# Kernel optimization log

Measured on AMD Instinct MI355X. Metric: run time of the kernel, lower is better.

Reference implementation:

```python
import jax, jax.numpy as jnp
import numpy as np

EPS = 1e-8  # torch F.cosine_similarity eps
TEMP = 1.0  # temperature k


def setup_inputs() -> dict:
    key = jax.random.key(0)
    k1, k2, k3 = jax.random.split(key, 3)
    B, T, N, D = 16, 4096, 512, 512
    c = jax.random.normal(k1, (B, T, D), dtype=jnp.float32)
    y_t = jax.random.normal(k2, (B, T, D), dtype=jnp.float32)
    y_distraction = jax.random.normal(k3, (B, N, D), dtype=jnp.float32)
    return {"c": c, "y_t": y_t, "y_distraction": y_distraction}


def reference(c, y_t, y_distraction):
    # norms clamped at eps, matching torch F.cosine_similarity
    n_c = jnp.maximum(jnp.linalg.norm(c, axis=-1), EPS)            # [B,T]
    n_t = jnp.maximum(jnp.linalg.norm(y_t, axis=-1), EPS)          # [B,T]
    n_d = jnpp_norm = jnp.maximum(jnp.linalg.norm(y_distraction, axis=-1), EPS)  # [B,N]

    # positive similarity and exp
    q_t = jnp.exp(jnp.sum(y_t * c, axis=-1) / (n_t * n_c) / TEMP)  # [B,T]

    # distractor cosine similarities via einsum (avoids [B,T,N,D] broadcast)
    scores = jnp.einsum('btd,bnd->btn', c, y_distraction)          # [B,T,N]
    scores = scores / (n_c[:, :, None] * n_d[:, None, :])
    q_distraction = jnp.sum(jnp.exp(scores / TEMP), axis=2) + q_t  # [B,T]

    loss = -jnp.sum(jnp.log(q_t / q_distraction))                  # scalar
    return loss
```

## Files before the change

### kernel.cpp

```cpp
#include <hip/hip_runtime.h>
#include <hip/hip_bf16.h>

#define B_   16
#define T_   4096
#define N_   512
#define D_   512
#define EPSF 1e-8f

typedef __attribute__((ext_vector_type(8))) short bf16x8;
typedef __attribute__((ext_vector_type(4))) float f32x4;

__device__ __forceinline__ unsigned int pack2bf(float a, float b) {
  unsigned int ua = __float_as_uint(a);
  ua += 0x7fffu + ((ua >> 16) & 1u);
  unsigned int ub = __float_as_uint(b);
  ub += 0x7fffu + ((ub >> 16) & 1u);
  return (ua >> 16) | (ub & 0xffff0000u);
}

__device__ __forceinline__ void gload_lds16(const void* g, void* l) {
  __builtin_amdgcn_global_load_lds(
      (const __attribute__((address_space(1))) unsigned int*)g,
      (__attribute__((address_space(3))) unsigned int*)l, 16, 0, 0);
}

__global__ void rownorms_d(const float* __restrict__ yd,
                           float* __restrict__ inv_nd,
                           unsigned short* __restrict__ ydbf) {
  const int tid = threadIdx.x;
  const int g   = tid >> 4;
  const int t   = tid & 15;
  const int row = blockIdx.x * 16 + g;
  const float* dr = yd + (size_t)row * D_;
  unsigned short* ob = ydbf + (size_t)row * D_;

  float dd = 0.f;
#pragma unroll
  for (int k = 0; k < 8; ++k) {
    const int col = k * 64 + t * 4;
    float4 a = *(const float4*)(dr + col);
    dd += a.x * a.x + a.y * a.y + a.z * a.z + a.w * a.w;
    uint2 p;
    p.x = pack2bf(a.x, a.y);
    p.y = pack2bf(a.z, a.w);
    *(uint2*)(ob + col) = p;
  }
#pragma unroll
  for (int m = 1; m < 16; m <<= 1) dd += __shfl_xor(dd, m);
  if (t == 0) inv_nd[row] = 1.f / fmaxf(sqrtf(dd), EPSF);
}

__device__ __forceinline__ void stage_B(unsigned char* Bsbuf,
                                        const unsigned short* __restrict__ Bb,
                                        int k0, int tid) {
#pragma unroll
  for (int j = 0; j < 8; ++j) {
    const int g   = j * 512 + tid;
    const int row = g >> 3;
    const int sch = (g & 7) ^ (row & 7);
    gload_lds16(Bb + (size_t)row * D_ + k0 + (sch << 3), Bsbuf + (g << 4));
  }
}

__device__ __forceinline__ void load_AT(const float* __restrict__ Ab,
                                        const float* __restrict__ Tb,
                                        int k0, int tid,
                                        float4* va, float4* vb) {
#pragma unroll
  for (int j = 0; j < 4; ++j) {
    const int g   = j * 512 + tid;
    const int row = g >> 4;
    const int c4  = g & 15;
    const size_t off = (size_t)row * D_ + k0 + (c4 << 2);
    va[j] = *(const float4*)(Ab + off);
    vb[j] = *(const float4*)(Tb + off);
  }
}

__device__ __forceinline__ void writeA_stats(unsigned char* As,
                                             const float4* va, const float4* vb,
                                             int tid,
                                             float* cc, float* tt, float* ct) {
#pragma unroll
  for (int j = 0; j < 4; ++j) {
    const int g   = j * 512 + tid;
    const int row = g >> 4;
    const int c4  = g & 15;
    const int off = (row << 7) + ((((c4 >> 1) ^ (row & 7))) << 4) + ((c4 & 1) << 3);
    uint2 pa;
    pa.x = pack2bf(va[j].x, va[j].y);
    pa.y = pack2bf(va[j].z, va[j].w);
    *(uint2*)(As + off) = pa;
    cc[j] += va[j].x * va[j].x + va[j].y * va[j].y + va[j].z * va[j].z + va[j].w * va[j].w;
    tt[j] += vb[j].x * vb[j].x + vb[j].y * vb[j].y + vb[j].z * vb[j].z + vb[j].w * vb[j].w;
    ct[j] += va[j].x * vb[j].x + va[j].y * vb[j].y + va[j].z * vb[j].z + va[j].w * vb[j].w;
  }
}

__launch_bounds__(512, 2)
__global__ void fused_ct(const float* __restrict__ c,
                         const float* __restrict__ yt,
                         const unsigned short* __restrict__ ydbf,
                         const float* __restrict__ inv_nd,
                         float* __restrict__ rt,
                         float* __restrict__ S) {
  __shared__ __align__(16) unsigned char As[128 * 64 * 2];
  __shared__ __align__(16) unsigned char Bs[2][512 * 64 * 2];
  __shared__ float s_invc[128];
  __shared__ float s_invd[512];

  const int mt = blockIdx.x;
  const int b  = blockIdx.y;
  const int tid  = threadIdx.x;
  const int lane = tid & 63;
  const int w    = tid >> 6;
  const int wm   = w >> 2, wn = w & 3;

  const float* Ab = c  + ((size_t)b * T_ + (size_t)mt * 128) * D_;
  const float* Tb = yt + ((size_t)b * T_ + (size_t)mt * 128) * D_;
  const unsigned short* Bb = ydbf + (size_t)b * N_ * D_;

  float4 va[4], vb[4];
  float cc[4] = {0.f, 0.f, 0.f, 0.f};
  float tt[4] = {0.f, 0.f, 0.f, 0.f};
  float ct[4] = {0.f, 0.f, 0.f, 0.f};

  stage_B(Bs[0], Bb, 0, tid);
  load_AT(Ab, Tb, 0, tid, va, vb);
  s_invd[tid] = inv_nd[b * N_ + tid];
  writeA_stats(As, va, vb, tid, cc, tt, ct);
  __syncthreads();

  f32x4 acc[4][8] = {};
  int cur = 0;

  for (int k0i = 0; k0i < 8; ++k0i) {
    const bool more = (k0i < 7);
    if (more) {
      load_AT(Ab, Tb, (k0i + 1) * 64, tid, va, vb);
      stage_B(Bs[cur ^ 1], Bb, (k0i + 1) * 64, tid);
    }

#pragma unroll
    for (int ks = 0; ks < 2; ++ks) {
      bf16x8 af[4], bfr[8];
#pragma unroll
      for (int i = 0; i < 4; ++i) {
        const int ar  = wm * 64 + i * 16 + (lane & 15);
        const int ach = (ks * 4 + (lane >> 4)) ^ (ar & 7);
        af[i] = *(const bf16x8*)(As + (ar << 7) + (ach << 4));
      }
#pragma unroll
      for (int n = 0; n < 8; ++n) {
        const int br  = wn * 128 + n * 16 + (lane & 15);
        const int bch = (ks * 4 + (lane >> 4)) ^ (br & 7);
        bfr[n] = *(const bf16x8*)(Bs[cur] + (br << 7) + (bch << 4));
      }
#pragma unroll
      for (int mi = 0; mi < 4; ++mi)
#pragma unroll
        for (int ni = 0; ni < 8; ++ni)
          acc[mi][ni] = __builtin_amdgcn_mfma_f32_16x16x32_bf16(
              af[mi], bfr[ni], acc[mi][ni], 0, 0, 0);
    }

    __syncthreads();
    if (more) {
      writeA_stats(As, va, vb, tid, cc, tt, ct);
      __syncthreads();
    }
    cur ^= 1;
  }

#pragma unroll
  for (int j = 0; j < 4; ++j) {
#pragma unroll
    for (int m = 1; m < 16; m <<= 1) {
      cc[j] += __shfl_xor(cc[j], m);
      tt[j] += __shfl_xor(tt[j], m);
      ct[j] += __shfl_xor(ct[j], m);
    }
    if ((tid & 15) == 0) {
      const int row = j * 32 + (tid >> 4);
      const float nc = fmaxf(sqrtf(cc[j]), EPSF);
      const float nt = fmaxf(sqrtf(tt[j]), EPSF);
      s_invc[row] = 1.f / nc;
      rt[b * T_ + mt * 128 + row] = ct[j] / (nt * nc);
    }
  }
  __syncthreads();

  float invd[8];
#pragma unroll
  for (int ni = 0; ni < 8; ++ni)
    invd[ni] = s_invd[wn * 128 + ni * 16 + (lane & 15)];

#pragma unroll
  for (int mi = 0; mi < 4; ++mi) {
    const int t0l = wm * 64 + mi * 16 + ((lane >> 4) << 2);
#pragma unroll
    for (int r = 0; r < 4; ++r) {
      const float invc = s_invc[t0l + r];
      float s = 0.f;
#pragma unroll
      for (int ni = 0; ni < 8; ++ni)
        s += __expf(acc[mi][ni][r] * invc * invd[ni]);
      s += __shfl_xor(s, 1);
      s += __shfl_xor(s, 2);
      s += __shfl_xor(s, 4);
      s += __shfl_xor(s, 8);
      if ((lane & 15) == 0)
        atomicAdd(&S[b * T_ + mt * 128 + t0l + r], s);
    }
  }
}

__global__ void final_loss(const float* __restrict__ S,
                           const float* __restrict__ rt,
                           float* __restrict__ out) {
  const int tid = threadIdx.x;
  float sum = 0.f;
  for (int i = blockIdx.x * blockDim.x + tid; i < B_ * T_;
       i += gridDim.x * blockDim.x) {
    const float r = rt[i];
    sum += logf(S[i] + __expf(r)) - r;
  }
#pragma unroll
  for (int m = 32; m; m >>= 1) sum += __shfl_xor(sum, m);
  __shared__ float ws[4];
  if ((tid & 63) == 0) ws[tid >> 6] = sum;
  __syncthreads();
  if (tid == 0) atomicAdd(out, ws[0] + ws[1] + ws[2] + ws[3]);
}

extern "C" void kernel_launch(void* const* d_in, const int* in_sizes, int n_in,
                              void* d_out, int out_size, void* d_ws, size_t ws_size,
                              hipStream_t stream) {
  (void)in_sizes; (void)n_in; (void)out_size; (void)ws_size;
  const float* c  = (const float*)d_in[0];
  const float* yt = (const float*)d_in[1];
  const float* yd = (const float*)d_in[2];
  float* out = (float*)d_out;

  const size_t ydbf_n = (size_t)B_ * N_ * D_;
  unsigned short* ydbf = (unsigned short*)d_ws;
  float* rt     = (float*)(ydbf + ydbf_n);
  float* inv_nd = rt + B_ * T_;
  float* S      = inv_nd + B_ * N_;

  hipMemsetAsync(S, 0, (size_t)B_ * T_ * sizeof(float), stream);
  hipMemsetAsync(out, 0, sizeof(float), stream);

  rownorms_d<<<B_ * N_ / 16, 256, 0, stream>>>(yd, inv_nd, ydbf);

  dim3 gF(T_ / 128, B_);
  fused_ct<<<gF, 512, 0, stream>>>(c, yt, ydbf, inv_nd, rt, S);

  final_loss<<<64, 256, 0, stream>>>(S, rt, out);
}
```

Before: 93.04 us.

## Pipeline K loop with 4-stage B and 3-stage A LDS buffers using K=32 tiles

Shrinks the K-tile from 64 to 32 and replaces the double-buffered loop with a deeper pipeline: four LDS stages for the distractor tile and three for the c tile, with loads issued two steps ahead. Each step now uses one barrier plus an explicit vmcnt/lgkmcnt wait instead of two __syncthreads, and the LDS swizzle is reworked for 64-byte rows. The aim is to hide global-load latency and cut barrier stalls, at the cost of more iterations, more register pressure for two sets of prefetched A/T values, and reliance on hand-counted wait counts being correct.

Result: slower. 110.5 us (+18.7%).

```diff
diff --git a/kernel.cpp b/kernel.cpp
--- a/kernel.cpp
+++ b/kernel.cpp
@@ -9,6 +9,8 @@
 
 typedef __attribute__((ext_vector_type(8))) short bf16x8;
 typedef __attribute__((ext_vector_type(4))) float f32x4;
+
+#define MEMFENCE asm volatile("" ::: "memory")
 
 __device__ __forceinline__ unsigned int pack2bf(float a, float b) {
   unsigned int ua = __float_as_uint(a);
@@ -50,43 +52,45 @@
   if (t == 0) inv_nd[row] = 1.f / fmaxf(sqrtf(dd), EPSF);
 }
 
-__device__ __forceinline__ void stage_B(unsigned char* Bsbuf,
-                                        const unsigned short* __restrict__ Bb,
-                                        int k0, int tid) {
-#pragma unroll
-  for (int j = 0; j < 8; ++j) {
+__device__ __forceinline__ void stage_B32(unsigned char* buf,
+                                          const unsigned short* __restrict__ Bb,
+                                          int k0, int tid) {
+#pragma unroll
+  for (int j = 0; j < 4; ++j) {
     const int g   = j * 512 + tid;
-    const int row = g >> 3;
-    const int sch = (g & 7) ^ (row & 7);
-    gload_lds16(Bb + (size_t)row * D_ + k0 + (sch << 3), Bsbuf + (g << 4));
-  }
-}
-
-__device__ __forceinline__ void load_AT(const float* __restrict__ Ab,
+    const int row = g >> 2;
+    const int x   = (row ^ (row >> 2)) & 3;
+    const int sch = (g & 3) ^ x;
+    gload_lds16(Bb + (size_t)row * D_ + k0 + (sch << 3), buf + (g << 4));
+  }
+}
+
+__device__ __forceinline__ void loadA32(const float* __restrict__ Ab,
                                         const float* __restrict__ Tb,
                                         int k0, int tid,
                                         float4* va, float4* vb) {
 #pragma unroll
-  for (int j = 0; j < 4; ++j) {
+  for (int j = 0; j < 2; ++j) {
     const int g   = j * 512 + tid;
-    const int row = g >> 4;
-    const int c4  = g & 15;
+    const int row = g >> 3;
+    const int c4  = g & 7;
     const size_t off = (size_t)row * D_ + k0 + (c4 << 2);
     va[j] = *(const float4*)(Ab + off);
     vb[j] = *(const float4*)(Tb + off);
   }
 }
 
-__device__ __forceinline__ void writeA_stats(unsigned char* As,
-                                             const float4* va, const float4* vb,
-                                             int tid,
-                                             float* cc, float* tt, float* ct) {
-#pragma unroll
-  for (int j = 0; j < 4; ++j) {
+__device__ __forceinline__ void writeA32(unsigned char* As,
+                                         const float4* va, const float4* vb,
+                                         int tid,
+                                         float* cc, float* tt, float* ct) {
+#pragma unroll
+  for (int j = 0; j < 2; ++j) {
     const int g   = j * 512 + tid;
-    const int row = g >> 4;
-    const int c4  = g & 15;
-    const int off = (row << 7) + ((((c4 >> 1) ^ (row & 7))) << 4) + ((c4 & 1) << 3);
+    const int row = g >> 3;
+    const int c4  = g & 7;
+    const int x   = (row ^ (row >> 2)) & 3;
+    const int off = (row << 6) + ((((c4 >> 1) ^ x)) << 4) + ((c4 & 1) << 3);
     uint2 pa;
     pa.x = pack2bf(va[j].x, va[j].y);
     pa.y = pack2bf(va[j].z, va[j].w);
@@ -97,6 +101,32 @@
   }
 }
 
+__device__ __forceinline__ void compute32(const unsigned char* As,
+                                          const unsigned char* Bs,
+                                          int wm, int wn, int lane,
+                                          f32x4 acc[4][8]) {
+  const int kc = lane >> 4;
+  bf16x8 af[4], bfr[8];
+#pragma unroll
+  for (int i = 0; i < 4; ++i) {
+    const int ar = wm * 64 + i * 16 + (lane & 15);
+    const int x  = (ar ^ (ar >> 2)) & 3;
+    af[i] = *(const bf16x8*)(As + (ar << 6) + ((kc ^ x) << 4));
+  }
+#pragma unroll
+  for (int n = 0; n < 8; ++n) {
+    const int br = wn * 128 + n * 16 + (lane & 15);
+    const int x  = (br ^ (br >> 2)) & 3;
+    bfr[n] = *(const bf16x8*)(Bs + (br << 6) + ((kc ^ x) << 4));
+  }
+#pragma unroll
+  for (int mi = 0; mi < 4; ++mi)
+#pragma unroll
+    for (int ni = 0; ni < 8; ++ni)
+      acc[mi][ni] = __builtin_amdgcn_mfma_f32_16x16x32_bf16(
+          af[mi], bfr[ni], acc[mi][ni], 0, 0, 0);
+}
+
 __launch_bounds__(512, 2)
 __global__ void fused_ct(const float* __restrict__ c,
                          const float* __restrict__ yt,
@@ -104,8 +134,8 @@
                          const float* __restrict__ inv_nd,
                          float* __restrict__ rt,
                          float* __restrict__ S) {
-  __shared__ __align__(16) unsigned char As[128 * 64 * 2];
-  __shared__ __align__(16) unsigned char Bs[2][512 * 64 * 2];
+  __shared__ __align__(16) unsigned char Bs[4][512 * 32 * 2];
+  __shared__ __align__(16) unsigned char As[3][128 * 32 * 2];
   __shared__ float s_invc[128];
   __shared__ float s_invd[512];
 
@@ -120,68 +150,62 @@
   const float* Tb = yt + ((size_t)b * T_ + (size_t)mt * 128) * D_;
   const unsigned short* Bb = ydbf + (size_t)b * N_ * D_;
 
-  float4 va[4], vb[4];
-  float cc[4] = {0.f, 0.f, 0.f, 0.f};
-  float tt[4] = {0.f, 0.f, 0.f, 0.f};
-  float ct[4] = {0.f, 0.f, 0.f, 0.f};
-
-  stage_B(Bs[0], Bb, 0, tid);
-  load_AT(Ab, Tb, 0, tid, va, vb);
+  float4 va0[2], vb0[2], va1[2], vb1[2];
+  float cc[2] = {0.f, 0.f}, tt[2] = {0.f, 0.f}, ct[2] = {0.f, 0.f};
+
+  stage_B32(Bs[0], Bb, 0, tid);
+  stage_B32(Bs[1], Bb, 32, tid);
+  loadA32(Ab, Tb, 0, tid, va0, vb0);
+  loadA32(Ab, Tb, 32, tid, va1, vb1);
   s_invd[tid] = inv_nd[b * N_ + tid];
-  writeA_stats(As, va, vb, tid, cc, tt, ct);
-  __syncthreads();
+  writeA32(As[0], va0, vb0, tid, cc, tt, ct);
 
   f32x4 acc[4][8] = {};
-  int cur = 0;
-
-  for (int k0i = 0; k0i < 8; ++k0i) {
-    const bool more = (k0i < 7);
-    if (more) {
-      load_AT(Ab, Tb, (k0i + 1) * 64, tid, va, vb);
-      stage_B(Bs[cur ^ 1], Bb, (k0i + 1) * 64, tid);
-    }
-
-#pragma unroll
-    for (int ks = 0; ks < 2; ++ks) {
-      bf16x8 af[4], bfr[8];
-#pragma unroll
-      for (int i = 0; i < 4; ++i) {
-        const int ar  = wm * 64 + i * 16 + (lane & 15);
-        const int ach = (ks * 4 + (lane >> 4)) ^ (ar & 7);
-        af[i] = *(const bf16x8*)(As + (ar << 7) + (ach << 4));
-      }
-#pragma unroll
-      for (int n = 0; n < 8; ++n) {
-        const int br  = wn * 128 + n * 16 + (lane & 15);
-        const int bch = (ks * 4 + (lane >> 4)) ^ (br & 7);
-        bfr[n] = *(const bf16x8*)(Bs[cur] + (br << 7) + (bch << 4));
-      }
-#pragma unroll
-      for (int mi = 0; mi < 4; ++mi)
-#pragma unroll
-        for (int ni = 0; ni < 8; ++ni)
-          acc[mi][ni] = __builtin_amdgcn_mfma_f32_16x16x32_bf16(
-              af[mi], bfr[ni], acc[mi][ni], 0, 0, 0);
-    }
-
-    __syncthreads();
-    if (more) {
-      writeA_stats(As, va, vb, tid, cc, tt, ct);
-      __syncthreads();
-    }
-    cur ^= 1;
-  }
-
-#pragma unroll
-  for (int j = 0; j < 4; ++j) {
-#pragma unroll
-    for (int m = 1; m < 16; m <<= 1) {
+  int asC = 0, asW = 1;
+
+  int t = 0;
+#pragma unroll 1
+  for (int tp = 0; tp < 7; ++tp) {
+    stage_B32(Bs[(t + 2) & 3], Bb, (t + 2) * 32, tid);
+    loadA32(Ab, Tb, (t + 2) * 32, tid, va0, vb0);
+    writeA32(As[asW], va1, vb1, tid, cc, tt, ct);
+    asm volatile("s_waitcnt vmcnt(8) lgkmcnt(0)" ::: "memory");
+    __builtin_amdgcn_s_barrier();
+    MEMFENCE;
+    compute32(As[asC], Bs[t & 3], wm, wn, lane, acc);
+    { int nW = 3 - asC - asW; asC = asW; asW = nW; }
+    ++t;
+    stage_B32(Bs[(t + 2) & 3], Bb, (t + 2) * 32, tid);
+    loadA32(Ab, Tb, (t + 2) * 32, tid, va1, vb1);
+    writeA32(As[asW], va0, vb0, tid, cc, tt, ct);
+    asm volatile("s_waitcnt vmcnt(8) lgkmcnt(0)" ::: "memory");
+    __builtin_amdgcn_s_barrier();
+    MEMFENCE;
+    compute32(As[asC], Bs[t & 3], wm, wn, lane, acc);
+    { int nW = 3 - asC - asW; asC = asW; asW = nW; }
+    ++t;
+  }
+  writeA32(As[asW], va1, vb1, tid, cc, tt, ct);
+  asm volatile("s_waitcnt vmcnt(4) lgkmcnt(0)" ::: "memory");
+  __builtin_amdgcn_s_barrier();
+  MEMFENCE;
+  compute32(As[asC], Bs[2], wm, wn, lane, acc);
+  { int nW = 3 - asC - asW; asC = asW; asW = nW; }
+  asm volatile("s_waitcnt vmcnt(0) lgkmcnt(0)" ::: "memory");
+  __builtin_amdgcn_s_barrier();
+  MEMFENCE;
+  compute32(As[asC], Bs[3], wm, wn, lane, acc);
+
+#pragma unroll
+  for (int j = 0; j < 2; ++j) {
+#pragma unroll
+    for (int m = 1; m < 8; m <<= 1) {
       cc[j] += __shfl_xor(cc[j], m);
       tt[j] += __shfl_xor(tt[j], m);
       ct[j] += __shfl_xor(ct[j], m);
     }
-    if ((tid & 15) == 0) {
-      const int row = j * 32 + (tid >> 4);
+    if ((tid & 7) == 0) {
+      const int row = j * 64 + (tid >> 3);
       const float nc = fmaxf(sqrtf(cc[j]), EPSF);
       const float nt = fmaxf(sqrtf(tt[j]), EPSF);
       s_invc[row] = 1.f / nc;
```

## Shrink fused tile to 32 rows with 256 threads and single-buffered B

Applied to the files above, without the earlier changes.

Changes the fused cosine/GEMM kernel from 128-row tiles with 512 threads and double-buffered B staging to 32-row tiles with 256 threads and one B buffer in LDS. B staging now happens after the compute barrier instead of overlapping with compute. The grid grows fourfold, meant to help occupancy and load balance. In exchange, each block reloads the whole 512x512 bf16 distractor matrix for only 32 rows, so B traffic per output rises fourfold, and the B loads are no longer hidden behind the MFMAs.

Measured after the change: 123.4 us. 1.33x slower.

```diff
diff --git a/kernel.cpp b/kernel.cpp
--- a/kernel.cpp
+++ b/kernel.cpp
@@ -50,63 +50,16 @@
   if (t == 0) inv_nd[row] = 1.f / fmaxf(sqrtf(dd), EPSF);
 }
 
-__device__ __forceinline__ void stage_B(unsigned char* Bsbuf,
-                                        const unsigned short* __restrict__ Bb,
-                                        int k0, int tid) {
-#pragma unroll
-  for (int j = 0; j < 8; ++j) {
-    const int g   = j * 512 + tid;
-    const int row = g >> 3;
-    const int sch = (g & 7) ^ (row & 7);
-    gload_lds16(Bb + (size_t)row * D_ + k0 + (sch << 3), Bsbuf + (g << 4));
-  }
-}
-
-__device__ __forceinline__ void load_AT(const float* __restrict__ Ab,
-                                        const float* __restrict__ Tb,
-                                        int k0, int tid,
-                                        float4* va, float4* vb) {
-#pragma unroll
-  for (int j = 0; j < 4; ++j) {
-    const int g   = j * 512 + tid;
-    const int row = g >> 4;
-    const int c4  = g & 15;
-    const size_t off = (size_t)row * D_ + k0 + (c4 << 2);
-    va[j] = *(const float4*)(Ab + off);
-    vb[j] = *(const float4*)(Tb + off);
-  }
-}
-
-__device__ __forceinline__ void writeA_stats(unsigned char* As,
-                                             const float4* va, const float4* vb,
-                                             int tid,
-                                             float* cc, float* tt, float* ct) {
-#pragma unroll
-  for (int j = 0; j < 4; ++j) {
-    const int g   = j * 512 + tid;
-    const int row = g >> 4;
-    const int c4  = g & 15;
-    const int off = (row << 7) + ((((c4 >> 1) ^ (row & 7))) << 4) + ((c4 & 1) << 3);
-    uint2 pa;
-    pa.x = pack2bf(va[j].x, va[j].y);
-    pa.y = pack2bf(va[j].z, va[j].w);
-    *(uint2*)(As + off) = pa;
-    cc[j] += va[j].x * va[j].x + va[j].y * va[j].y + va[j].z * va[j].z + va[j].w * va[j].w;
-    tt[j] += vb[j].x * vb[j].x + vb[j].y * vb[j].y + vb[j].z * vb[j].z + vb[j].w * vb[j].w;
-    ct[j] += va[j].x * vb[j].x + va[j].y * vb[j].y + va[j].z * vb[j].z + va[j].w * vb[j].w;
-  }
-}
-
-__launch_bounds__(512, 2)
+__launch_bounds__(256, 2)
 __global__ void fused_ct(const float* __restrict__ c,
                          const float* __restrict__ yt,
                          const unsigned short* __restrict__ ydbf,
                          const float* __restrict__ inv_nd,
                          float* __restrict__ rt,
                          float* __restrict__ S) {
-  __shared__ __align__(16) unsigned char As[128 * 64 * 2];
-  __shared__ __align__(16) unsigned char Bs[2][512 * 64 * 2];
-  __shared__ float s_invc[128];
+  __shared__ __align__(16) unsigned char Bs[512 * 64 * 2];
+  __shared__ __align__(16) unsigned char As[32 * 64 * 2];
+  __shared__ float s_invc[32];
   __shared__ float s_invd[512];
 
   const int mt = blockIdx.x;
@@ -114,50 +67,79 @@
   const int tid  = threadIdx.x;
   const int lane = tid & 63;
   const int w    = tid >> 6;
-  const int wm   = w >> 2, wn = w & 3;
-
-  const float* Ab = c  + ((size_t)b * T_ + (size_t)mt * 128) * D_;
-  const float* Tb = yt + ((size_t)b * T_ + (size_t)mt * 128) * D_;
+
+  const float* Ab = c  + ((size_t)b * T_ + (size_t)mt * 32) * D_;
+  const float* Tb = yt + ((size_t)b * T_ + (size_t)mt * 32) * D_;
   const unsigned short* Bb = ydbf + (size_t)b * N_ * D_;
 
-  float4 va[4], vb[4];
-  float cc[4] = {0.f, 0.f, 0.f, 0.f};
-  float tt[4] = {0.f, 0.f, 0.f, 0.f};
-  float ct[4] = {0.f, 0.f, 0.f, 0.f};
-
-  stage_B(Bs[0], Bb, 0, tid);
-  load_AT(Ab, Tb, 0, tid, va, vb);
+  float4 va[2], vb[2];
+  float cc[2] = {0.f, 0.f}, tt[2] = {0.f, 0.f}, ct[2] = {0.f, 0.f};
+
+  auto loadA = [&](int k0) {
+#pragma unroll
+    for (int j = 0; j < 2; ++j) {
+      const int g   = j * 256 + tid;
+      const int row = g >> 4;
+      const int c4  = g & 15;
+      const size_t off = (size_t)row * D_ + k0 + (c4 << 2);
+      va[j] = *(const float4*)(Ab + off);
+      vb[j] = *(const float4*)(Tb + off);
+    }
+  };
+  auto writeA = [&]() {
+#pragma unroll
+    for (int j = 0; j < 2; ++j) {
+      const int g   = j * 256 + tid;
+      const int row = g >> 4;
+      const int c4  = g & 15;
+      const int off = (row << 7) + ((((c4 >> 1) ^ (row & 7))) << 4) + ((c4 & 1) << 3);
+      uint2 pa;
+      pa.x = pack2bf(va[j].x, va[j].y);
+      pa.y = pack2bf(va[j].z, va[j].w);
+      *(uint2*)(As + off) = pa;
+      cc[j] += va[j].x * va[j].x + va[j].y * va[j].y + va[j].z * va[j].z + va[j].w * va[j].w;
+      tt[j] += vb[j].x * vb[j].x + vb[j].y * vb[j].y + vb[j].z * vb[j].z + vb[j].w * vb[j].w;
+      ct[j] += va[j].x * vb[j].x + va[j].y * vb[j].y + va[j].z * vb[j].z + va[j].w * vb[j].w;
+    }
+  };
+  auto stageB = [&](int k0) {
+#pragma unroll
+    for (int j = 0; j < 16; ++j) {
+      const int g   = j * 256 + tid;
+      const int row = g >> 3;
+      const int sch = (g & 7) ^ (row & 7);
+      gload_lds16(Bb + (size_t)row * D_ + k0 + (sch << 3), Bs + (g << 4));
+    }
+  };
+
+  loadA(0);
+  stageB(0);
   s_invd[tid] = inv_nd[b * N_ + tid];
-  writeA_stats(As, va, vb, tid, cc, tt, ct);
+  s_invd[tid + 256] = inv_nd[b * N_ + tid + 256];
+  writeA();
   __syncthreads();
 
-  f32x4 acc[4][8] = {};
-  int cur = 0;
-
-  for (int k0i = 0; k0i < 8; ++k0i) {
-    const bool more = (k0i < 7);
-    if (more) {
-      load_AT(Ab, Tb, (k0i + 1) * 64, tid, va, vb);
-      stage_B(Bs[cur ^ 1], Bb, (k0i + 1) * 64, tid);
-    }
+  f32x4 acc[2][8] = {};
+
+  for (int t = 0; t < 8; ++t) {
+    if (t < 7) loadA((t + 1) * 64);
 
 #pragma unroll
     for (int ks = 0; ks < 2; ++ks) {
-      bf16x8 af[4], bfr[8];
-#pragma unroll
-      for (int i = 0; i < 4; ++i) {
-        const int ar  = wm * 64 + i * 16 + (lane & 15);
-        const int ach = (ks * 4 + (lane >> 4)) ^ (ar & 7);
-        af[i] = *(const bf16x8*)(As + (ar << 7) + (ach << 4));
+      const int kc = ks * 4 + (lane >> 4);
+      bf16x8 af[2], bfr[8];
+#pragma unroll
+      for (int i = 0; i < 2; ++i) {
+        const int ar = i * 16 + (lane & 15);
+        af[i] = *(const bf16x8*)(As + (ar << 7) + ((kc ^ (ar & 7)) << 4));
       }
 #pragma unroll
       for (int n = 0; n < 8; ++n) {
-        const int br  = wn * 128 + n * 16 + (lane & 15);
-        const int bch = (ks * 4 + (lane >> 4)) ^ (br & 7);
-        bfr[n] = *(const bf16x8*)(Bs[cur] + (br << 7) + (bch << 4));
+        const int br = w * 128 + n * 16 + (lane & 15);
+        bfr[n] = *(const bf16x8*)(Bs + (br << 7) + ((kc ^ (br & 7)) << 4));
       }
 #pragma unroll
-      for (int mi = 0; mi < 4; ++mi)
+      for (int mi = 0; mi < 2; ++mi)
 #pragma unroll
         for (int ni = 0; ni < 8; ++ni)
           acc[mi][ni] = __builtin_amdgcn_mfma_f32_16x16x32_bf16(
@@ -165,15 +147,15 @@
     }
 
     __syncthreads();
-    if (more) {
-      writeA_stats(As, va, vb, tid, cc, tt, ct);
+    if (t < 7) {
+      stageB((t + 1) * 64);
+      writeA();
       __syncthreads();
     }
-    cur ^= 1;
-  }
-
-#pragma unroll
-  for (int j = 0; j < 4; ++j) {
+  }
+
+#pragma unroll
+  for (int j = 0; j < 2; ++j) {
 #pragma unroll
     for (int m = 1; m < 16; m <<= 1) {
       cc[j] += __shfl_xor(cc[j], m);
@@ -181,11 +163,11 @@
       ct[j] += __shfl_xor(ct[j], m);
     }
     if ((tid & 15) == 0) {
-      const int row = j * 32 + (tid >> 4);
+      const int row = j * 16 + (tid >> 4);
       const float nc = fmaxf(sqrtf(cc[j]), EPSF);
       const float nt = fmaxf(sqrtf(tt[j]), EPSF);
       s_invc[row] = 1.f / nc;
-      rt[b * T_ + mt * 128 + row] = ct[j] / (nt * nc);
+      rt[b * T_ + mt * 32 + row] = ct[j] / (nt * nc);
     }
   }
   __syncthreads();
@@ -193,11 +175,11 @@
   float invd[8];
 #pragma unroll
   for (int ni = 0; ni < 8; ++ni)
-    invd[ni] = s_invd[wn * 128 + ni * 16 + (lane & 15)];
-
-#pragma unroll
-  for (int mi = 0; mi < 4; ++mi) {
-    const int t0l = wm * 64 + mi * 16 + ((lane >> 4) << 2);
+    invd[ni] = s_invd[w * 128 + ni * 16 + (lane & 15)];
+
+#pragma unroll
+  for (int mi = 0; mi < 2; ++mi) {
+    const int t0l = mi * 16 + ((lane >> 4) << 2);
 #pragma unroll
     for (int r = 0; r < 4; ++r) {
       const float invc = s_invc[t0l + r];
@@ -210,7 +192,7 @@
       s += __shfl_xor(s, 4);
       s += __shfl_xor(s, 8);
       if ((lane & 15) == 0)
-        atomicAdd(&S[b * T_ + mt * 128 + t0l + r], s);
+        atomicAdd(&S[b * T_ + mt * 32 + t0l + r], s);
     }
   }
 }
@@ -253,8 +235,8 @@
 
   rownorms_d<<<B_ * N_ / 16, 256, 0, stream>>>(yd, inv_nd, ydbf);
 
-  dim3 gF(T_ / 128, B_);
-  fused_ct<<<gF, 512, 0, stream>>>(c, yt, ydbf, inv_nd, rt, S);
+  dim3 gF(T_ / 32, B_);
+  fused_ct<<<gF, 256, 0, stream>>>(c, yt, ydbf, inv_nd, rt, S);
 
   final_loss<<<64, 256, 0, stream>>>(S, rt, out);
 }
```
